# Performance work log

Hardware: AMD Instinct MI355X
Metric: run time of the kernel (lower is better)

## Reference

```python
import jax, jax.numpy as jnp
import numpy as np

NUM_BUSES = 20000
NUM_LINES = 320000
OTHER = 1000
BATCH = 128


def setup_inputs() -> dict:
    key = jax.random.key(0)
    k1, k2, k3, k4, k5 = jax.random.split(key, 5)
    x = jax.random.normal(k1, (BATCH, 2 * NUM_BUSES + OTHER), dtype=jnp.float32)
    from_indices = jax.random.randint(k2, (NUM_LINES,), 0, NUM_BUSES, dtype=jnp.int32)
    to_indices = jax.random.randint(k3, (NUM_LINES,), 0, NUM_BUSES, dtype=jnp.int32)
    # reactances bounded away from 0 (realistic p.u. line reactances)
    reactances = 0.01 + 0.2 * jax.random.uniform(k4, (NUM_LINES,), dtype=jnp.float32)
    limits = 0.5 + 1.5 * jax.random.uniform(k5, (NUM_LINES,), dtype=jnp.float32)
    return {
        "x": x,
        "from_indices": from_indices,
        "to_indices": to_indices,
        "reactances": reactances,
        "limits": limits,
        "num_buses": NUM_BUSES,
    }


def reference(x, from_indices, to_indices, reactances, limits, num_buses):
    nb = num_buses
    voltages = x[:, :nb]                     # [B, nb]
    angles = x[:, nb:2 * nb]                 # [B, nb]
    other_params = x[:, 2 * nb:]             # [B, other]

    from_a = angles[:, from_indices]         # [B, L] gather
    to_a = angles[:, to_indices]
    angle_diffs = from_a - to_a
    flows = angle_diffs / reactances[None, :]
    over = jnp.abs(flows / limits[None, :]) > 1.0

    # Torch runs this branch only if any line is over limit; when none are,
    # adjustments are identically zero, so applying unconditionally is exact.
    required = jnp.sign(angle_diffs) * (reactances * limits)[None, :]
    adjustments = jnp.where(over, required, angle_diffs) - angle_diffs  # [B, L]
    half = adjustments * 0.5
    # angles = angles + from_adjustments - to_adjustments
    #        = angles + scatter_add(from, adj/2) + scatter_add(to, adj/2)
    # (torch accumulates -adj/2 into to_adjustments, then subtracts it)
    delta = jnp.zeros_like(angles).at[:, from_indices].add(half).at[:, to_indices].add(half)
    angles2 = angles + delta

    diffs2 = angles2[:, from_indices] - angles2[:, to_indices]
    flows2 = diffs2 / reactances[None, :]

    out = jnp.concatenate([voltages, angles2, other_params], axis=1)
    return out, flows2
```

## Files before the change

### kernel.cpp

```cpp
#include <hip/hip_runtime.h>

#define NB     20000
#define NL     320000
#define NOTH   1000
#define BATCH  128
#define ROW    (2*NB + NOTH)
#define CAP    80
#define NBLK   256
#define LSEG   (NL/NBLK)
#define BCHUNK 8
#define CB     (NB/BCHUNK)
#define NSLICE 4
#define LPS    (NL/NSLICE)

#define SCANB  40
#define COPYB  256
#define CPF4   (BATCH*(NB/4 + NOTH/4))

typedef float vf4 __attribute__((ext_vector_type(4)));

__device__ __forceinline__ float fast_rcp(float a)
{
    float r;
    asm volatile("v_rcp_f32 %0, %1" : "=v"(r) : "v"(a));
    return r;
}

__global__ __launch_bounds__(512) void histo_k(
    const int* __restrict__ fidx, const int* __restrict__ tidx,
    ushort* __restrict__ H)
{
    extern __shared__ uint h[];
    for (int i = threadIdx.x; i < NB; i += 512) h[i] = 0u;
    __syncthreads();

    const int l0 = blockIdx.x * LSEG;
    for (int l = l0 + (int)threadIdx.x; l < l0 + LSEG; l += 512) {
        atomicAdd(&h[fidx[l]], 1u);
        atomicAdd(&h[tidx[l]], 1u);
    }
    __syncthreads();

    ushort* __restrict__ Hrow = H + (size_t)blockIdx.x * NB;
    for (int i = threadIdx.x; i < NB / 2; i += 512) {
        ushort2 u; u.x = (ushort)h[2 * i]; u.y = (ushort)h[2 * i + 1];
        ((ushort2*)Hrow)[i] = u;
    }
}

__global__ __launch_bounds__(512) void scancopy_k(
    ushort* __restrict__ H, int* __restrict__ cnt,
    const float* __restrict__ x, float* __restrict__ out)
{
    if (blockIdx.x < SCANB) {
        const int u = blockIdx.x * 512 + threadIdx.x;
        if (u >= NB) return;
        uint run = 0;
        for (int b = 0; b < NBLK; ++b) {
            const uint v = H[(size_t)b * NB + u];
            H[(size_t)b * NB + u] = (ushort)run;
            run += v;
        }
        cnt[u] = (int)run;
    } else {
        const int nthr = COPYB * 512;
        int idx = (blockIdx.x - SCANB) * 512 + threadIdx.x;
        for (; idx < CPF4; idx += nthr) {
            const int b = idx / (NB / 4 + NOTH / 4);
            const int r = idx % (NB / 4 + NOTH / 4);
            const int off = (r < NB / 4) ? r : (2 * NB / 4) + (r - NB / 4);
            const size_t p = (size_t)b * (ROW / 4) + off;
            ((float4*)out)[p] = ((const float4*)x)[p];
        }
    }
}

__global__ __launch_bounds__(512) void place_k(
    const int* __restrict__ fidx, const int* __restrict__ tidx,
    const float* __restrict__ xr, const float* __restrict__ lim,
    const ushort* __restrict__ H, unsigned* __restrict__ bins)
{
    extern __shared__ char sm[];
    uint*   __restrict__ h    = (uint*)sm;
    ushort* __restrict__ pref = (ushort*)(sm + NB * 4);

    const ushort* __restrict__ Hrow = H + (size_t)blockIdx.x * NB;
    for (int i = threadIdx.x; i < NB; i += 512) h[i] = 0u;
    for (int i = threadIdx.x; i < NB / 2; i += 512)
        ((ushort2*)pref)[i] = ((const ushort2*)Hrow)[i];
    __syncthreads();

    const int l0 = blockIdx.x * LSEG;
    for (int l = l0 + (int)threadIdx.x; l < l0 + LSEG; l += 512) {
        const int fi = fidx[l];
        const int ti = tidx[l];
        union { float f; unsigned u; } c; c.f = xr[l] * lim[l];
        const unsigned rl16 = (c.u + 0x8000u) >> 16;

        const uint s0 = (uint)pref[fi] + atomicAdd(&h[fi], 1u);
        if (s0 < CAP) bins[(size_t)s0 * NB + fi] = ((unsigned)ti << 17) | rl16;
        const uint s1 = (uint)pref[ti] + atomicAdd(&h[ti], 1u);
        if (s1 < CAP) bins[(size_t)s1 * NB + ti] =
            ((unsigned)fi << 17) | (1u << 16) | rl16;
    }
}

__global__ __launch_bounds__(1024) void delta_k(
    const float* __restrict__ x, const int* __restrict__ cnt,
    const unsigned* __restrict__ bins, float* __restrict__ out)
{
    extern __shared__ float a[];
    const int b  = blockIdx.x % BATCH;
    const int cb = blockIdx.x / BATCH;

    const float* __restrict__ xrow = x   + (size_t)b * ROW;
    float*       __restrict__ orow = out + (size_t)b * ROW;

    for (int i = threadIdx.x; i < NB / 4; i += 1024)
        ((float4*)a)[i] = ((const float4*)(xrow + NB))[i];
    __syncthreads();

    const int base = cb * CB;
    for (int bus = base + (int)threadIdx.x; bus < base + CB; bus += 1024) {
        const int   n  = min(cnt[bus], CAP);
        const float ab = a[bus];
        float ds = 0.0f;
        int k = 0;
        #define CONTRIB(W)                                                   \
        {                                                                    \
            const unsigned w  = (W);                                         \
            const int   other = (int)(w >> 17);                              \
            const float rl    = __uint_as_float((w & 0xFFFFu) << 16);        \
            const float ad    = ab - a[other];                               \
            if (fabsf(ad) > rl) {                                            \
                float hh = 0.5f * (copysignf(rl, ad) - ad);                  \
                if (w & (1u << 16)) hh = -hh;                                \
                ds += hh;                                                    \
            }                                                                \
        }
        for (; k + 4 <= n; k += 4) {
            const unsigned w0 = bins[(size_t)(k + 0) * NB + bus];
            const unsigned w1 = bins[(size_t)(k + 1) * NB + bus];
            const unsigned w2 = bins[(size_t)(k + 2) * NB + bus];
            const unsigned w3 = bins[(size_t)(k + 3) * NB + bus];
            CONTRIB(w0) CONTRIB(w1) CONTRIB(w2) CONTRIB(w3)
        }
        for (; k < n; ++k) CONTRIB(bins[(size_t)k * NB + bus])
        #undef CONTRIB
        orow[NB + bus] = ab + ds;
    }
}

__global__ __launch_bounds__(1024) void flows_lds_k(
    const float* __restrict__ out, const int* __restrict__ fidx,
    const int* __restrict__ tidx, const float* __restrict__ xr,
    float* __restrict__ f2)
{
    extern __shared__ float a2[];
    const int b = blockIdx.x % BATCH;
    const int s = blockIdx.x / BATCH;

    const float* __restrict__ src = out + (size_t)b * ROW + NB;
    for (int i = threadIdx.x; i < NB / 4; i += 1024)
        ((float4*)a2)[i] = ((const float4*)src)[i];
    __syncthreads();

    float* __restrict__ frow = f2 + (size_t)b * NL;
    const int q0 = s * (LPS / 4);
    const int q1 = q0 + (LPS / 4);
    for (int q = q0 + (int)threadIdx.x; q < q1; q += 1024) {
        const int4   f = ((const int4*)fidx)[q];
        const int4   t = ((const int4*)tidx)[q];
        const float4 r = ((const float4*)xr)[q];
        vf4 o;
        o.x = (a2[f.x] - a2[t.x]) * fast_rcp(r.x);
        o.y = (a2[f.y] - a2[t.y]) * fast_rcp(r.y);
        o.z = (a2[f.z] - a2[t.z]) * fast_rcp(r.z);
        o.w = (a2[f.w] - a2[t.w]) * fast_rcp(r.w);
        __builtin_nontemporal_store(o, &((vf4*)frow)[q]);
    }
}

extern "C" void kernel_launch(void* const* d_in, const int* in_sizes, int n_in,
                              void* d_out, int out_size, void* d_ws, size_t ws_size,
                              hipStream_t stream)
{
    const float* x   = (const float*)d_in[0];
    const int*   fi  = (const int*)  d_in[1];
    const int*   ti  = (const int*)  d_in[2];
    const float* xr  = (const float*)d_in[3];
    const float* lim = (const float*)d_in[4];

    float* out    = (float*)d_out;
    float* flows2 = out + (size_t)BATCH * ROW;

    const size_t hBytes = (size_t)NBLK * NB * sizeof(ushort);
    ushort*   H    = (ushort*)d_ws;
    int*      cnt  = (int*)((char*)d_ws + hBytes);
    unsigned* bins = (unsigned*)((char*)d_ws + hBytes + (size_t)NB * 4);

    histo_k<<<dim3(NBLK), dim3(512), NB * sizeof(uint), stream>>>(fi, ti, H);

    scancopy_k<<<dim3(SCANB + COPYB), dim3(512), 0, stream>>>(H, cnt, x, out);

    place_k<<<dim3(NBLK), dim3(512),
              NB * sizeof(uint) + NB * sizeof(ushort), stream>>>(
        fi, ti, xr, lim, H, bins);

    delta_k<<<dim3(BCHUNK * BATCH), dim3(1024), NB * sizeof(float), stream>>>(
        x, cnt, bins, out);

    flows_lds_k<<<dim3(NSLICE * BATCH), dim3(1024), NB * sizeof(float), stream>>>(
        out, fi, ti, xr, flows2);
}
```

Before: 119.4 us.

## Pack line endpoints and reciprocal reactance into uint2, shrink histogram to bytes

A new set of blocks is added to the histogram kernel. They pack from/to indices into one 32-bit word and store the precomputed reciprocal reactance beside it, so the flows kernel reads 8 bytes per line instead of 12 and skips the reciprocal. The per-block histogram and prefix arrays drop from ushort to uchar, with counts clamped at 255. The bus-chunk and slice counts are also halved. The byte prefix could wrap if a bus's total degree exceeds 255, which is unlikely at this degree distribution.

```diff
diff --git a/kernel.cpp b/kernel.cpp
--- a/kernel.cpp
+++ b/kernel.cpp
@@ -8,11 +8,11 @@
 #define CAP    80
 #define NBLK   256
 #define LSEG   (NL/NBLK)
-#define BCHUNK 8
+#define PACKB  64
+#define BCHUNK 4
 #define CB     (NB/BCHUNK)
-#define NSLICE 4
+#define NSLICE 2
 #define LPS    (NL/NSLICE)
-
 #define SCANB  40
 #define COPYB  256
 #define CPF4   (BATCH*(NB/4 + NOTH/4))
@@ -26,10 +26,21 @@
     return r;
 }
 
-__global__ __launch_bounds__(512) void histo_k(
+__global__ __launch_bounds__(512) void histo_pack_k(
     const int* __restrict__ fidx, const int* __restrict__ tidx,
-    ushort* __restrict__ H)
-{
+    const float* __restrict__ xr, uchar* __restrict__ H,
+    uint2* __restrict__ ldata)
+{
+    if (blockIdx.x >= NBLK) {
+        const int gt = (blockIdx.x - NBLK) * 512 + (int)threadIdx.x;
+        for (int l = gt; l < NL; l += PACKB * 512) {
+            uint2 w;
+            w.x = ((unsigned)fidx[l] << 15) | (unsigned)tidx[l];
+            w.y = __float_as_uint(1.0f / xr[l]);
+            ldata[l] = w;
+        }
+        return;
+    }
     extern __shared__ uint h[];
     for (int i = threadIdx.x; i < NB; i += 512) h[i] = 0u;
     __syncthreads();
@@ -41,30 +52,31 @@
     }
     __syncthreads();
 
-    ushort* __restrict__ Hrow = H + (size_t)blockIdx.x * NB;
-    for (int i = threadIdx.x; i < NB / 2; i += 512) {
-        ushort2 u; u.x = (ushort)h[2 * i]; u.y = (ushort)h[2 * i + 1];
-        ((ushort2*)Hrow)[i] = u;
+    uint* __restrict__ Hrow = (uint*)(H + (size_t)blockIdx.x * NB);
+    for (int i = threadIdx.x; i < NB / 4; i += 512) {
+        const uint c0 = min(h[4 * i + 0], 255u), c1 = min(h[4 * i + 1], 255u);
+        const uint c2 = min(h[4 * i + 2], 255u), c3 = min(h[4 * i + 3], 255u);
+        Hrow[i] = c0 | (c1 << 8) | (c2 << 16) | (c3 << 24);
     }
 }
 
 __global__ __launch_bounds__(512) void scancopy_k(
-    ushort* __restrict__ H, int* __restrict__ cnt,
+    uchar* __restrict__ H, int* __restrict__ cnt,
     const float* __restrict__ x, float* __restrict__ out)
 {
     if (blockIdx.x < SCANB) {
-        const int u = blockIdx.x * 512 + threadIdx.x;
+        const int u = blockIdx.x * 512 + (int)threadIdx.x;
         if (u >= NB) return;
         uint run = 0;
         for (int b = 0; b < NBLK; ++b) {
             const uint v = H[(size_t)b * NB + u];
-            H[(size_t)b * NB + u] = (ushort)run;
+            H[(size_t)b * NB + u] = (uchar)run;
             run += v;
         }
         cnt[u] = (int)run;
     } else {
         const int nthr = COPYB * 512;
-        int idx = (blockIdx.x - SCANB) * 512 + threadIdx.x;
+        int idx = (blockIdx.x - SCANB) * 512 + (int)threadIdx.x;
         for (; idx < CPF4; idx += nthr) {
             const int b = idx / (NB / 4 + NOTH / 4);
             const int r = idx % (NB / 4 + NOTH / 4);
@@ -78,16 +90,16 @@
 __global__ __launch_bounds__(512) void place_k(
     const int* __restrict__ fidx, const int* __restrict__ tidx,
     const float* __restrict__ xr, const float* __restrict__ lim,
-    const ushort* __restrict__ H, unsigned* __restrict__ bins)
+    const uchar* __restrict__ H, unsigned* __restrict__ bins)
 {
     extern __shared__ char sm[];
-    uint*   __restrict__ h    = (uint*)sm;
-    ushort* __restrict__ pref = (ushort*)(sm + NB * 4);
-
-    const ushort* __restrict__ Hrow = H + (size_t)blockIdx.x * NB;
+    uint*  __restrict__ h    = (uint*)sm;
+    uchar* __restrict__ pref = (uchar*)(sm + NB * 4);
+
+    const uchar* __restrict__ Hrow = H + (size_t)blockIdx.x * NB;
     for (int i = threadIdx.x; i < NB; i += 512) h[i] = 0u;
-    for (int i = threadIdx.x; i < NB / 2; i += 512)
-        ((ushort2*)pref)[i] = ((const ushort2*)Hrow)[i];
+    for (int i = threadIdx.x; i < NB / 16; i += 512)
+        ((uint4*)pref)[i] = ((const uint4*)Hrow)[i];
     __syncthreads();
 
     const int l0 = blockIdx.x * LSEG;
@@ -151,9 +163,8 @@
     }
 }
 
-__global__ __launch_bounds__(1024) void flows_lds_k(
-    const float* __restrict__ out, const int* __restrict__ fidx,
-    const int* __restrict__ tidx, const float* __restrict__ xr,
+__global__ __launch_bounds__(1024) void flows_k(
+    const float* __restrict__ out, const uint2* __restrict__ ldata,
     float* __restrict__ f2)
 {
     extern __shared__ float a2[];
@@ -169,14 +180,13 @@
     const int q0 = s * (LPS / 4);
     const int q1 = q0 + (LPS / 4);
     for (int q = q0 + (int)threadIdx.x; q < q1; q += 1024) {
-        const int4   f = ((const int4*)fidx)[q];
-        const int4   t = ((const int4*)tidx)[q];
-        const float4 r = ((const float4*)xr)[q];
+        const uint4 p0 = ((const uint4*)ldata)[2 * q];
+        const uint4 p1 = ((const uint4*)ldata)[2 * q + 1];
         vf4 o;
-        o.x = (a2[f.x] - a2[t.x]) * fast_rcp(r.x);
-        o.y = (a2[f.y] - a2[t.y]) * fast_rcp(r.y);
-        o.z = (a2[f.z] - a2[t.z]) * fast_rcp(r.z);
-        o.w = (a2[f.w] - a2[t.w]) * fast_rcp(r.w);
+        o.x = (a2[p0.x >> 15] - a2[p0.x & 0x7FFFu]) * __uint_as_float(p0.y);
+        o.y = (a2[p0.z >> 15] - a2[p0.z & 0x7FFFu]) * __uint_as_float(p0.w);
+        o.z = (a2[p1.x >> 15] - a2[p1.x & 0x7FFFu]) * __uint_as_float(p1.y);
+        o.w = (a2[p1.z >> 15] - a2[p1.z & 0x7FFFu]) * __uint_as_float(p1.w);
         __builtin_nontemporal_store(o, &((vf4*)frow)[q]);
     }
 }
@@ -194,22 +204,22 @@
     float* out    = (float*)d_out;
     float* flows2 = out + (size_t)BATCH * ROW;
 
-    const size_t hBytes = (size_t)NBLK * NB * sizeof(ushort);
-    ushort*   H    = (ushort*)d_ws;
-    int*      cnt  = (int*)((char*)d_ws + hBytes);
-    unsigned* bins = (unsigned*)((char*)d_ws + hBytes + (size_t)NB * 4);
-
-    histo_k<<<dim3(NBLK), dim3(512), NB * sizeof(uint), stream>>>(fi, ti, H);
+    uchar*    H     = (uchar*)d_ws;
+    int*      cnt   = (int*)((char*)d_ws + (size_t)NBLK * NB);
+    unsigned* bins  = (unsigned*)((char*)cnt + (size_t)NB * 4);
+    uint2*    ldata = (uint2*)((char*)bins + (size_t)CAP * NB * 4);
+
+    histo_pack_k<<<dim3(NBLK + PACKB), dim3(512), NB * sizeof(uint), stream>>>(
+        fi, ti, xr, H, ldata);
 
     scancopy_k<<<dim3(SCANB + COPYB), dim3(512), 0, stream>>>(H, cnt, x, out);
 
-    place_k<<<dim3(NBLK), dim3(512),
-              NB * sizeof(uint) + NB * sizeof(ushort), stream>>>(
+    place_k<<<dim3(NBLK), dim3(512), NB * 4 + NB, stream>>>(
         fi, ti, xr, lim, H, bins);
 
     delta_k<<<dim3(BCHUNK * BATCH), dim3(1024), NB * sizeof(float), stream>>>(
         x, cnt, bins, out);
 
-    flows_lds_k<<<dim3(NSLICE * BATCH), dim3(1024), NB * sizeof(float), stream>>>(
-        out, fi, ti, xr, flows2);
-}
+    flows_k<<<dim3(NSLICE * BATCH), dim3(1024), NB * sizeof(float), stream>>>(
+        out, ldata, flows2);
+}
```

Measured after the change: 120.9 us. Within noise of the previous version (+1.3%).

## Fold passthrough copy into delta kernel and shrink histogram to bytes

Applied to the files above, without the earlier changes.

The voltage and other-parameter passthrough copy moves out of the scan kernel and into the delta kernel, so each block copies its own bus chunk while it already holds the row. This leaves the scan as a small standalone kernel. Per-block histogram counts and prefixes are stored as clamped 8-bit values instead of 16-bit, which halves the histogram traffic in the scan and place kernels. The flows kernel now uses 2 slices instead of 4 and plain float4 stores instead of nontemporal ones. The 8-bit prefixes assume no bus ever reaches 255 incident lines.

```diff
diff --git a/kernel.cpp b/kernel.cpp
--- a/kernel.cpp
+++ b/kernel.cpp
@@ -10,14 +10,8 @@
 #define LSEG   (NL/NBLK)
 #define BCHUNK 8
 #define CB     (NB/BCHUNK)
-#define NSLICE 4
+#define NSLICE 2
 #define LPS    (NL/NSLICE)
-
-#define SCANB  40
-#define COPYB  256
-#define CPF4   (BATCH*(NB/4 + NOTH/4))
-
-typedef float vf4 __attribute__((ext_vector_type(4)));
 
 __device__ __forceinline__ float fast_rcp(float a)
 {
@@ -28,7 +22,7 @@
 
 __global__ __launch_bounds__(512) void histo_k(
     const int* __restrict__ fidx, const int* __restrict__ tidx,
-    ushort* __restrict__ H)
+    uchar* __restrict__ H)
 {
     extern __shared__ uint h[];
     for (int i = threadIdx.x; i < NB; i += 512) h[i] = 0u;
@@ -41,53 +35,41 @@
     }
     __syncthreads();
 
-    ushort* __restrict__ Hrow = H + (size_t)blockIdx.x * NB;
-    for (int i = threadIdx.x; i < NB / 2; i += 512) {
-        ushort2 u; u.x = (ushort)h[2 * i]; u.y = (ushort)h[2 * i + 1];
-        ((ushort2*)Hrow)[i] = u;
-    }
-}
-
-__global__ __launch_bounds__(512) void scancopy_k(
-    ushort* __restrict__ H, int* __restrict__ cnt,
-    const float* __restrict__ x, float* __restrict__ out)
-{
-    if (blockIdx.x < SCANB) {
-        const int u = blockIdx.x * 512 + threadIdx.x;
-        if (u >= NB) return;
-        uint run = 0;
-        for (int b = 0; b < NBLK; ++b) {
-            const uint v = H[(size_t)b * NB + u];
-            H[(size_t)b * NB + u] = (ushort)run;
-            run += v;
-        }
-        cnt[u] = (int)run;
-    } else {
-        const int nthr = COPYB * 512;
-        int idx = (blockIdx.x - SCANB) * 512 + threadIdx.x;
-        for (; idx < CPF4; idx += nthr) {
-            const int b = idx / (NB / 4 + NOTH / 4);
-            const int r = idx % (NB / 4 + NOTH / 4);
-            const int off = (r < NB / 4) ? r : (2 * NB / 4) + (r - NB / 4);
-            const size_t p = (size_t)b * (ROW / 4) + off;
-            ((float4*)out)[p] = ((const float4*)x)[p];
-        }
-    }
+    uint* __restrict__ Hrow = (uint*)(H + (size_t)blockIdx.x * NB);
+    for (int i = threadIdx.x; i < NB / 4; i += 512) {
+        const uint c0 = min(h[4 * i + 0], 255u), c1 = min(h[4 * i + 1], 255u);
+        const uint c2 = min(h[4 * i + 2], 255u), c3 = min(h[4 * i + 3], 255u);
+        Hrow[i] = c0 | (c1 << 8) | (c2 << 16) | (c3 << 24);
+    }
+}
+
+__global__ __launch_bounds__(512) void scan_k(
+    uchar* __restrict__ H, int* __restrict__ cnt)
+{
+    const int u = blockIdx.x * 512 + (int)threadIdx.x;
+    if (u >= NB) return;
+    uint run = 0;
+    for (int b = 0; b < NBLK; ++b) {
+        const uint v = H[(size_t)b * NB + u];
+        H[(size_t)b * NB + u] = (uchar)run;
+        run += v;
+    }
+    cnt[u] = (int)run;
 }
 
 __global__ __launch_bounds__(512) void place_k(
     const int* __restrict__ fidx, const int* __restrict__ tidx,
     const float* __restrict__ xr, const float* __restrict__ lim,
-    const ushort* __restrict__ H, unsigned* __restrict__ bins)
+    const uchar* __restrict__ H, unsigned* __restrict__ bins)
 {
     extern __shared__ char sm[];
-    uint*   __restrict__ h    = (uint*)sm;
-    ushort* __restrict__ pref = (ushort*)(sm + NB * 4);
-
-    const ushort* __restrict__ Hrow = H + (size_t)blockIdx.x * NB;
+    uint*  __restrict__ h    = (uint*)sm;
+    uchar* __restrict__ pref = (uchar*)(sm + NB * 4);
+
+    const uchar* __restrict__ Hrow = H + (size_t)blockIdx.x * NB;
     for (int i = threadIdx.x; i < NB; i += 512) h[i] = 0u;
-    for (int i = threadIdx.x; i < NB / 2; i += 512)
-        ((ushort2*)pref)[i] = ((const ushort2*)Hrow)[i];
+    for (int i = threadIdx.x; i < NB / 16; i += 512)
+        ((uint4*)pref)[i] = ((const uint4*)Hrow)[i];
     __syncthreads();
 
     const int l0 = blockIdx.x * LSEG;
@@ -105,7 +87,7 @@
     }
 }
 
-__global__ __launch_bounds__(1024) void delta_k(
+__global__ __launch_bounds__(1024) void delta_copy_k(
     const float* __restrict__ x, const int* __restrict__ cnt,
     const unsigned* __restrict__ bins, float* __restrict__ out)
 {
@@ -119,6 +101,12 @@
     for (int i = threadIdx.x; i < NB / 4; i += 1024)
         ((float4*)a)[i] = ((const float4*)(xrow + NB))[i];
     __syncthreads();
+
+    for (int i = threadIdx.x; i < CB / 4; i += 1024)
+        ((float4*)(orow + cb * CB))[i] = ((const float4*)(xrow + cb * CB))[i];
+    if (cb == 0)
+        for (int i = threadIdx.x; i < NOTH / 4; i += 1024)
+            ((float4*)(orow + 2 * NB))[i] = ((const float4*)(xrow + 2 * NB))[i];
 
     const int base = cb * CB;
     for (int bus = base + (int)threadIdx.x; bus < base + CB; bus += 1024) {
@@ -172,12 +160,12 @@
         const int4   f = ((const int4*)fidx)[q];
         const int4   t = ((const int4*)tidx)[q];
         const float4 r = ((const float4*)xr)[q];
-        vf4 o;
+        float4 o;
         o.x = (a2[f.x] - a2[t.x]) * fast_rcp(r.x);
         o.y = (a2[f.y] - a2[t.y]) * fast_rcp(r.y);
         o.z = (a2[f.z] - a2[t.z]) * fast_rcp(r.z);
         o.w = (a2[f.w] - a2[t.w]) * fast_rcp(r.w);
-        __builtin_nontemporal_store(o, &((vf4*)frow)[q]);
+        ((float4*)frow)[q] = o;
     }
 }
 
@@ -194,20 +182,18 @@
     float* out    = (float*)d_out;
     float* flows2 = out + (size_t)BATCH * ROW;
 
-    const size_t hBytes = (size_t)NBLK * NB * sizeof(ushort);
-    ushort*   H    = (ushort*)d_ws;
-    int*      cnt  = (int*)((char*)d_ws + hBytes);
-    unsigned* bins = (unsigned*)((char*)d_ws + hBytes + (size_t)NB * 4);
+    uchar*    H    = (uchar*)d_ws;
+    int*      cnt  = (int*)((char*)d_ws + (size_t)NBLK * NB);
+    unsigned* bins = (unsigned*)((char*)cnt + (size_t)NB * 4);
 
     histo_k<<<dim3(NBLK), dim3(512), NB * sizeof(uint), stream>>>(fi, ti, H);
 
-    scancopy_k<<<dim3(SCANB + COPYB), dim3(512), 0, stream>>>(H, cnt, x, out);
-
-    place_k<<<dim3(NBLK), dim3(512),
-              NB * sizeof(uint) + NB * sizeof(ushort), stream>>>(
+    scan_k<<<dim3((NB + 511) / 512), dim3(512), 0, stream>>>(H, cnt);
+
+    place_k<<<dim3(NBLK), dim3(512), NB * 4 + NB, stream>>>(
         fi, ti, xr, lim, H, bins);
 
-    delta_k<<<dim3(BCHUNK * BATCH), dim3(1024), NB * sizeof(float), stream>>>(
+    delta_copy_k<<<dim3(BCHUNK * BATCH), dim3(1024), NB * sizeof(float), stream>>>(
         x, cnt, bins, out);
 
     flows_lds_k<<<dim3(NSLICE * BATCH), dim3(1024), NB * sizeof(float), stream>>>(
```

New measurement: 113.7 us. 1.05x faster.
